# Performance work log

Measured on AMD Instinct MI355X. Metric: run time of the kernel, lower is better.

Reference implementation:

```python
import jax, jax.numpy as jnp
import numpy as np

H = 1024      # hidden_size
I = 512       # moe_intermediate_size
E = 8         # n_routed_experts
K = 2         # num_experts_per_tok
SI = I * 2    # shared expert intermediate (n_shared_experts=2)
B, S = 2, 1024


def setup_inputs() -> dict:
    key = jax.random.key(0)
    ks = jax.random.split(key, 9)
    s = 0.02
    return {
        "x": jax.random.normal(ks[0], (B, S, H), jnp.float32),
        "gate_w": jax.random.normal(ks[1], (E, H), jnp.float32) * s,
        "lb_bias": jnp.zeros((E,), jnp.float32),
        "expert_gate_w": jax.random.normal(ks[2], (E, I, H), jnp.float32) * s,
        "expert_up_w": jax.random.normal(ks[3], (E, I, H), jnp.float32) * s,
        "expert_down_w": jax.random.normal(ks[4], (E, H, I), jnp.float32) * s,
        "shared_gate_w": jax.random.normal(ks[5], (SI, H), jnp.float32) * s,
        "shared_up_w": jax.random.normal(ks[6], (SI, H), jnp.float32) * s,
        "shared_down_w": jax.random.normal(ks[7], (H, SI), jnp.float32) * s,
    }


def _mlp(x, gw, uw, dw):
    # SwiGLU: down( silu(gate(x)) * up(x) )
    return (jax.nn.silu(x @ gw.T) * (x @ uw.T)) @ dw.T


def reference(x, gate_w, lb_bias, expert_gate_w, expert_up_w, expert_down_w,
              shared_gate_w, shared_up_w, shared_down_w):
    b, s, h = x.shape
    xf = x.reshape(-1, h)                                   # [T, H]
    # --- SimpleRouter (sigmoid scoring) ---
    logits = xf @ gate_w.T + lb_bias                        # [T, E]
    scores = jax.nn.sigmoid(logits.astype(jnp.float32))
    topw, topi = jax.lax.top_k(scores, K)                   # [T, K]
    topw = (topw / (topw.sum(-1, keepdims=True) + 1e-8)).astype(x.dtype)
    # --- _process_local: per-expert dispatch/compute/combine ---
    # Faithful to torch source: expert_weights[mask].mean(dim=-1) collapses to a
    # SCALAR per expert (mean routing weight over all tokens sent to that expert).
    out = jnp.zeros_like(xf)
    for e in range(E):
        m = (topi == e)                                     # [T, K]
        sel = m.any(axis=-1)                                # [T]
        cnt = m.sum()
        wmean = (topw * m).sum() / jnp.maximum(cnt, 1).astype(topw.dtype)
        y = _mlp(xf, expert_gate_w[e], expert_up_w[e], expert_down_w[e])  # [T, H]
        out = out + jnp.where(sel[:, None], y * wmean, jnp.zeros((), x.dtype))
    out = out.reshape(b, s, h)
    # --- shared experts ---
    out = out + _mlp(x, shared_gate_w, shared_up_w, shared_down_w)
    return out
```

## Files before the change

### kernel.cpp

```cpp
#include <hip/hip_runtime.h>

#define H_DIM 1024
#define I_DIM 512
#define NE 8
#define SI_DIM 1024
#define NT 2048

typedef __bf16 bf16;
typedef __bf16 bf16x4 __attribute__((ext_vector_type(4)));
typedef __bf16 bf16x8 __attribute__((ext_vector_type(8)));
typedef float f32x4 __attribute__((ext_vector_type(4)));

#define W_GU 0ull
#define W_DN 8388608ull
#define W_SGU 12582912ull
#define W_SDN 14680064ull
#define W_TOT 15728640ull

#define NWB 15360
#define NRB 512

#define OFF_CNT 0
#define OFF_WM 64
#define OFF_TOPI 1024
#define OFF_TOPW (OFF_TOPI + NT * 8)
#define OFF_LISTS (OFF_TOPW + NT * 8)
#define OFF_WB (OFF_LISTS + NE * NT * 4)
#define OFF_XB (OFF_WB + (size_t)W_TOT * 2)
#define OFF_ACTE (OFF_XB + (size_t)NT * H_DIM * 2)
#define OFF_ACTS (OFF_ACTE + (size_t)NE * NT * I_DIM * 2)

__device__ __forceinline__ bf16x4 cvt4(f32x4 v) {
  bf16x4 r;
  r.x = (bf16)v.x; r.y = (bf16)v.y; r.z = (bf16)v.z; r.w = (bf16)v.w;
  return r;
}

__device__ __forceinline__ void glds16(const bf16* g, bf16* l) {
  __builtin_amdgcn_global_load_lds(
      (const __attribute__((address_space(1))) unsigned int*)g,
      (__attribute__((address_space(3))) unsigned int*)l, 16, 0, 0);
}

__global__ __launch_bounds__(256) void prep_kernel(
    const float* __restrict__ x, const float* __restrict__ gw,
    const float* __restrict__ lb, const float* __restrict__ eg,
    const float* __restrict__ eu, const float* __restrict__ ed,
    const float* __restrict__ sg, const float* __restrict__ su,
    const float* __restrict__ sd, bf16* __restrict__ wb,
    bf16* __restrict__ xb, int2* __restrict__ topi,
    float2* __restrict__ topw) {
  const int bx = blockIdx.x;
  const int tid = threadIdx.x;
  if (bx < NWB) {
    size_t i = ((size_t)bx * 256 + tid) * 4;
    const float* src;
    if (i < W_DN) {
      size_t z = i >> 20;
      int rem = (int)(i & ((1u << 20) - 1));
      int rp = rem >> 10, k = rem & 1023;
      int b = rp >> 4;
      int sr = ((b >> 1) << 4) | (rp & 15);
      src = ((b & 1) ? eu : eg) + (z << 19) + ((size_t)sr << 10) + k;
    } else if (i < W_SGU) {
      src = ed + (i - W_DN);
    } else if (i < W_SDN) {
      int rem = (int)(i - W_SGU);
      int rp = rem >> 10, k = rem & 1023;
      int b = rp >> 4;
      int sr = ((b >> 1) << 4) | (rp & 15);
      src = ((b & 1) ? su : sg) + ((size_t)sr << 10) + k;
    } else {
      src = sd + (i - W_SDN);
    }
    *(bf16x4*)(wb + i) = cvt4(*(const f32x4*)src);
  } else {
    const int lane = tid & 63;
    const int t = (bx - NWB) * 4 + (tid >> 6);
    const float* xr = x + (size_t)t * H_DIM;
    bf16* xw = xb + (size_t)t * H_DIM;
    float s[NE];
#pragma unroll
    for (int e = 0; e < NE; e++) s[e] = 0.f;
#pragma unroll
    for (int k0 = 0; k0 < H_DIM; k0 += 256) {
      f32x4 xv = *(const f32x4*)(xr + k0 + lane * 4);
      *(bf16x4*)(xw + k0 + lane * 4) = cvt4(xv);
#pragma unroll
      for (int e = 0; e < NE; e++) {
        f32x4 gv = *(const f32x4*)(gw + e * H_DIM + k0 + lane * 4);
        s[e] += xv.x * gv.x + xv.y * gv.y + xv.z * gv.z + xv.w * gv.w;
      }
    }
#pragma unroll
    for (int e = 0; e < NE; e++) {
      float v = s[e];
#pragma unroll
      for (int off = 32; off > 0; off >>= 1) v += __shfl_xor(v, off);
      s[e] = v;
    }
    if (lane == 0) {
      float sc[NE];
#pragma unroll
      for (int e = 0; e < NE; e++) sc[e] = 1.f / (1.f + expf(-(s[e] + lb[e])));
      int i1 = 0;
#pragma unroll
      for (int e = 1; e < NE; e++)
        if (sc[e] > sc[i1]) i1 = e;
      int i2 = -1;
#pragma unroll
      for (int e = 0; e < NE; e++) {
        if (e == i1) continue;
        if (i2 < 0 || sc[e] > sc[i2]) i2 = e;
      }
      float w1 = sc[i1], w2 = sc[i2];
      float inv = 1.f / (w1 + w2 + 1e-8f);
      topi[t] = make_int2(i1, i2);
      topw[t] = make_float2(w1 * inv, w2 * inv);
    }
  }
}

__global__ __launch_bounds__(256) void build_kernel(
    const int2* __restrict__ topi, const float2* __restrict__ topw,
    int* __restrict__ cnt, float* __restrict__ wm, int* __restrict__ lists) {
  const int e = blockIdx.x;
  const int wave = threadIdx.x >> 6, lane = threadIdx.x & 63;
  __shared__ int wc[4];
  __shared__ float wf[4];
  const int tbeg = wave * (NT / 4), tend = tbeg + NT / 4;

  int c = 0;
  float wa = 0.f;
  for (int t0 = tbeg; t0 < tend; t0 += 64) {
    int2 ti = topi[t0 + lane];
    float2 tw = topw[t0 + lane];
    bool hit = (ti.x == e) || (ti.y == e);
    float w = (ti.x == e) ? tw.x : ((ti.y == e) ? tw.y : 0.f);
    c += __popcll(__ballot(hit));
#pragma unroll
    for (int off = 32; off > 0; off >>= 1) w += __shfl_xor(w, off);
    wa += w;
  }
  if (lane == 0) { wc[wave] = c; wf[wave] = wa; }
  __syncthreads();
  int pos = 0;
  for (int w = 0; w < wave; w++) pos += wc[w];
  for (int t0 = tbeg; t0 < tend; t0 += 64) {
    int t = t0 + lane;
    int2 ti = topi[t];
    bool hit = (ti.x == e) || (ti.y == e);
    unsigned long long m = __ballot(hit);
    int pre = __popcll(m & ((1ull << lane) - 1ull));
    if (hit) lists[e * NT + pos + pre] = t;
    pos += __popcll(m);
  }
  if (threadIdx.x == 0) {
    int ctot = wc[0] + wc[1] + wc[2] + wc[3];
    cnt[e] = ctot;
    wm[e] = (wf[0] + wf[1] + wf[2] + wf[3]) / (float)(ctot > 0 ? ctot : 1);
  }
}

__global__ __launch_bounds__(256, 4) void gemm_gu(
    const bf16* __restrict__ wb, const bf16* __restrict__ xb,
    const int* __restrict__ cnt, const int* __restrict__ lists,
    bf16* __restrict__ act_e, bf16* __restrict__ act_s) {
  const int z = blockIdx.z, ct = blockIdx.x, rt = blockIdx.y;
  const int tid = threadIdx.x;
  __shared__ int rows_s[64];
  __shared__ __align__(16) bf16 As[64 * 64];
  __shared__ __align__(16) bf16 Bs[128 * 64];
  int mrem, ldc;
  bf16* Cb;
  const bf16* Bb;
  if (z < NE) {
    if (ct >= 8) return;
    int c = cnt[z];
    if (rt * 64 >= c) return;
    mrem = c - rt * 64;
    if (tid < 64)
      rows_s[tid] = lists[z * NT + rt * 64 + (tid < mrem ? tid : mrem - 1)];
    Bb = wb + W_GU + ((size_t)z << 20) + (size_t)ct * 128 * H_DIM;
    Cb = act_e + ((size_t)z * NT + rt * 64) * I_DIM;
    ldc = I_DIM;
  } else {
    mrem = 64;
    if (tid < 64) rows_s[tid] = rt * 64 + tid;
    Bb = wb + W_SGU + (size_t)ct * 128 * H_DIM;
    Cb = act_s + (size_t)rt * 64 * SI_DIM;
    ldc = SI_DIM;
  }
  __syncthreads();

  const int lane = tid & 63, wave = tid >> 6;
  const int mw = (wave & 1) * 32, nw = (wave >> 1) * 64;
  const int l15 = lane & 15, quad = lane >> 4;
  const int srow = tid >> 3;
  const int cch = tid & 7;
  const int p8 = cch * 8;
  const int sx = (l15 & 7) * 8;

  const bf16 *ap[2], *bp[4];
  int alo[2], blo[4];
#pragma unroll
  for (int r = 0; r < 2; r++) {
    int R = srow + r * 32;
    int gs = (cch ^ (R & 7)) * 8;
    ap[r] = xb + (size_t)rows_s[R] * H_DIM + gs;
    alo[r] = R * 64 + p8;
  }
#pragma unroll
  for (int r = 0; r < 4; r++) {
    int R = srow + r * 32;
    int gs = (cch ^ (R & 7)) * 8;
    bp[r] = Bb + (size_t)R * H_DIM + gs;
    blo[r] = R * 64 + p8;
  }

  f32x4 acc[2][4] = {};
  for (int k0 = 0; k0 < H_DIM; k0 += 64) {
#pragma unroll
    for (int r = 0; r < 2; r++) glds16(ap[r] + k0, &As[alo[r]]);
#pragma unroll
    for (int r = 0; r < 4; r++) glds16(bp[r] + k0, &Bs[blo[r]]);
    __syncthreads();
#pragma unroll
    for (int kk = 0; kk < 2; kk++) {
      const int ko = (kk * 4 + quad) * 8;
      bf16x8 av[2], bv[4];
#pragma unroll
      for (int i = 0; i < 2; i++)
        av[i] = *(const bf16x8*)&As[(mw + i * 16 + l15) * 64 + (ko ^ sx)];
#pragma unroll
      for (int j = 0; j < 4; j++)
        bv[j] = *(const bf16x8*)&Bs[(nw + j * 16 + l15) * 64 + (ko ^ sx)];
#pragma unroll
      for (int i = 0; i < 2; i++)
#pragma unroll
        for (int j = 0; j < 4; j++)
          acc[i][j] = __builtin_amdgcn_mfma_f32_16x16x32_bf16(av[i], bv[j], acc[i][j], 0, 0, 0);
    }
    __syncthreads();
  }

#pragma unroll
  for (int i = 0; i < 2; i++) {
#pragma unroll
    for (int rg = 0; rg < 4; rg++) {
      int rl = mw + i * 16 + quad * 4 + rg;
      if (rl < mrem) {
#pragma unroll
        for (int jp = 0; jp < 2; jp++) {
          float g = acc[i][jp * 2][rg];
          float u = acc[i][jp * 2 + 1][rg];
          int c = ct * 64 + (nw >> 1) + jp * 16 + l15;
          Cb[(size_t)rl * ldc + c] = (bf16)((g / (1.f + __expf(-g))) * u);
        }
      }
    }
  }
}

__global__ __launch_bounds__(256, 4) void gemm_down(
    const bf16* __restrict__ wb, const bf16* __restrict__ act_e,
    const bf16* __restrict__ act_s, const int* __restrict__ cnt,
    const float* __restrict__ wm, const int* __restrict__ lists,
    float* __restrict__ out) {
  const int z = blockIdx.z, ct = blockIdx.x, rt = blockIdx.y;
  const int tid = threadIdx.x;
  __shared__ int rows_s[64];
  __shared__ __align__(16) bf16 As[64 * 64];
  __shared__ __align__(16) bf16 Bs[128 * 64];
  int K, mrem;
  const bf16 *Ab, *Bb;
  if (z < NE) {
    int c = cnt[z];
    if (rt * 64 >= c) return;
    mrem = c - rt * 64;
    if (tid < 64)
      rows_s[tid] = lists[z * NT + rt * 64 + (tid < mrem ? tid : mrem - 1)];
    Ab = act_e + ((size_t)z * NT + rt * 64) * I_DIM;
    K = I_DIM;
    Bb = wb + W_DN + ((size_t)z << 19) + (size_t)ct * 128 * I_DIM;
  } else {
    mrem = 64;
    if (tid < 64) rows_s[tid] = rt * 64 + tid;
    Ab = act_s + (size_t)rt * 64 * SI_DIM;
    K = SI_DIM;
    Bb = wb + W_SDN + (size_t)ct * 128 * SI_DIM;
  }
  __syncthreads();

  const int lane = tid & 63, wave = tid >> 6;
  const int mw = (wave & 1) * 32, nw = (wave >> 1) * 64;
  const int l15 = lane & 15, quad = lane >> 4;
  const int srow = tid >> 3;
  const int cch = tid & 7;
  const int p8 = cch * 8;
  const int sx = (l15 & 7) * 8;

  const bf16 *ap[2], *bp[4];
  int alo[2], blo[4];
#pragma unroll
  for (int r = 0; r < 2; r++) {
    int R = srow + r * 32;
    int gs = (cch ^ (R & 7)) * 8;
    ap[r] = Ab + (size_t)R * K + gs;
    alo[r] = R * 64 + p8;
  }
#pragma unroll
  for (int r = 0; r < 4; r++) {
    int R = srow + r * 32;
    int gs = (cch ^ (R & 7)) * 8;
    bp[r] = Bb + (size_t)R * K + gs;
    blo[r] = R * 64 + p8;
  }

  f32x4 acc[2][4] = {};
  for (int k0 = 0; k0 < K; k0 += 64) {
#pragma unroll
    for (int r = 0; r < 2; r++) glds16(ap[r] + k0, &As[alo[r]]);
#pragma unroll
    for (int r = 0; r < 4; r++) glds16(bp[r] + k0, &Bs[blo[r]]);
    __syncthreads();
#pragma unroll
    for (int kk = 0; kk < 2; kk++) {
      const int ko = (kk * 4 + quad) * 8;
      bf16x8 av[2], bv[4];
#pragma unroll
      for (int i = 0; i < 2; i++)
        av[i] = *(const bf16x8*)&As[(mw + i * 16 + l15) * 64 + (ko ^ sx)];
#pragma unroll
      for (int j = 0; j < 4; j++)
        bv[j] = *(const bf16x8*)&Bs[(nw + j * 16 + l15) * 64 + (ko ^ sx)];
#pragma unroll
      for (int i = 0; i < 2; i++)
#pragma unroll
        for (int j = 0; j < 4; j++)
          acc[i][j] = __builtin_amdgcn_mfma_f32_16x16x32_bf16(av[i], bv[j], acc[i][j], 0, 0, 0);
    }
    __syncthreads();
  }

  const float wsc = (z < NE) ? wm[z] : 1.f;
#pragma unroll
  for (int i = 0; i < 2; i++) {
#pragma unroll
    for (int rg = 0; rg < 4; rg++) {
      int rl = mw + i * 16 + quad * 4 + rg;
      if (rl < mrem) {
        int t = rows_s[rl];
        float* orow = out + (size_t)t * H_DIM + ct * 128 + nw;
#pragma unroll
        for (int j = 0; j < 4; j++)
          atomicAdd(&orow[j * 16 + l15], wsc * acc[i][j][rg]);
      }
    }
  }
}

extern "C" void kernel_launch(void* const* d_in, const int* in_sizes, int n_in,
                              void* d_out, int out_size, void* d_ws,
                              size_t ws_size, hipStream_t stream) {
  (void)in_sizes; (void)n_in; (void)out_size; (void)ws_size;
  const float* x  = (const float*)d_in[0];
  const float* gw = (const float*)d_in[1];
  const float* lb = (const float*)d_in[2];
  const float* eg = (const float*)d_in[3];
  const float* eu = (const float*)d_in[4];
  const float* ed = (const float*)d_in[5];
  const float* sg = (const float*)d_in[6];
  const float* su = (const float*)d_in[7];
  const float* sd = (const float*)d_in[8];
  float* out = (float*)d_out;
  char* ws = (char*)d_ws;

  int* cnt     = (int*)(ws + OFF_CNT);
  float* wm    = (float*)(ws + OFF_WM);
  int2* topi   = (int2*)(ws + OFF_TOPI);
  float2* topw = (float2*)(ws + OFF_TOPW);
  int* lists   = (int*)(ws + OFF_LISTS);
  bf16* wb     = (bf16*)(ws + OFF_WB);
  bf16* xb     = (bf16*)(ws + OFF_XB);
  bf16* act_e  = (bf16*)(ws + OFF_ACTE);
  bf16* act_s  = (bf16*)(ws + OFF_ACTS);

  hipMemsetAsync(d_out, 0, (size_t)NT * H_DIM * sizeof(float), stream);
  prep_kernel<<<NWB + NRB, 256, 0, stream>>>(x, gw, lb, eg, eu, ed, sg, su, sd,
                                             wb, xb, topi, topw);
  build_kernel<<<NE, 256, 0, stream>>>(topi, topw, cnt, wm, lists);
  gemm_gu<<<dim3(16, 32, 9), 256, 0, stream>>>(wb, xb, cnt, lists, act_e,
                                               act_s);
  gemm_down<<<dim3(8, 32, 9), 256, 0, stream>>>(wb, act_e, act_s, cnt, wm,
                                                lists, out);
}
```

Baseline: 203.3 us.

## Fuse all MoE stages into one persistent kernel with grid barriers

Replaces the memset plus four kernel launches with a single persistent kernel of 1024 blocks. The blocks loop over the prep, routing-list, gate/up GEMM and down GEMM work units and separate the phases with atomic global barriers. Output zeroing moves into the first phase. This removes launch gaps and tail effects between stages, but needs all 1024 blocks co-resident (256 CUs at 4 blocks each) or the barrier deadlocks. It also loses the dynamic early exit of empty tiles, which now cost a loop iteration.

```diff
diff --git a/kernel.cpp b/kernel.cpp
--- a/kernel.cpp
+++ b/kernel.cpp
@@ -5,6 +5,7 @@
 #define NE 8
 #define SI_DIM 1024
 #define NT 2048
+#define GRID 1024
 
 typedef __bf16 bf16;
 typedef __bf16 bf16x4 __attribute__((ext_vector_type(4)));
@@ -19,6 +20,8 @@
 
 #define NWB 15360
 #define NRB 512
+#define NZB 2048
+#define NU (NWB + NRB + NZB)
 
 #define OFF_CNT 0
 #define OFF_WM 64
@@ -29,6 +32,7 @@
 #define OFF_XB (OFF_WB + (size_t)W_TOT * 2)
 #define OFF_ACTE (OFF_XB + (size_t)NT * H_DIM * 2)
 #define OFF_ACTS (OFF_ACTE + (size_t)NE * NT * I_DIM * 2)
+#define OFF_BAR (OFF_ACTS + (size_t)NT * SI_DIM * 2)
 
 __device__ __forceinline__ bf16x4 cvt4(f32x4 v) {
   bf16x4 r;
@@ -42,156 +46,151 @@
       (__attribute__((address_space(3))) unsigned int*)l, 16, 0, 0);
 }
 
-__global__ __launch_bounds__(256) void prep_kernel(
+__device__ __forceinline__ void gsync(unsigned* bar) {
+  __syncthreads();
+  if (threadIdx.x == 0) {
+    __threadfence();
+    __hip_atomic_fetch_add(bar, 1u, __ATOMIC_RELAXED, __HIP_MEMORY_SCOPE_AGENT);
+    while (__hip_atomic_load(bar, __ATOMIC_RELAXED, __HIP_MEMORY_SCOPE_AGENT) <
+           (unsigned)GRID) {
+      __builtin_amdgcn_s_sleep(4);
+    }
+    __threadfence();
+  }
+  __syncthreads();
+}
+
+__global__ __launch_bounds__(256, 4) void moe_kernel(
     const float* __restrict__ x, const float* __restrict__ gw,
     const float* __restrict__ lb, const float* __restrict__ eg,
     const float* __restrict__ eu, const float* __restrict__ ed,
     const float* __restrict__ sg, const float* __restrict__ su,
     const float* __restrict__ sd, bf16* __restrict__ wb,
     bf16* __restrict__ xb, int2* __restrict__ topi,
-    float2* __restrict__ topw) {
-  const int bx = blockIdx.x;
+    float2* __restrict__ topw, int* __restrict__ cnt,
+    float* __restrict__ wm, int* __restrict__ lists,
+    bf16* __restrict__ act_e, bf16* __restrict__ act_s,
+    float* __restrict__ out, unsigned* __restrict__ bar) {
   const int tid = threadIdx.x;
-  if (bx < NWB) {
-    size_t i = ((size_t)bx * 256 + tid) * 4;
-    const float* src;
-    if (i < W_DN) {
-      size_t z = i >> 20;
-      int rem = (int)(i & ((1u << 20) - 1));
-      int rp = rem >> 10, k = rem & 1023;
-      int b = rp >> 4;
-      int sr = ((b >> 1) << 4) | (rp & 15);
-      src = ((b & 1) ? eu : eg) + (z << 19) + ((size_t)sr << 10) + k;
-    } else if (i < W_SGU) {
-      src = ed + (i - W_DN);
-    } else if (i < W_SDN) {
-      int rem = (int)(i - W_SGU);
-      int rp = rem >> 10, k = rem & 1023;
-      int b = rp >> 4;
-      int sr = ((b >> 1) << 4) | (rp & 15);
-      src = ((b & 1) ? su : sg) + ((size_t)sr << 10) + k;
+  const int bid = blockIdx.x;
+  __shared__ __align__(16) char smem[24832];
+  bf16* As = (bf16*)smem;
+  bf16* Bs = (bf16*)(smem + 8192);
+  int* rows_s = (int*)(smem + 24576);
+
+  for (int u = bid; u < NU; u += GRID) {
+    if (u < NWB) {
+      size_t i = ((size_t)u * 256 + tid) * 4;
+      const float* src;
+      if (i < W_DN) {
+        size_t z = i >> 20;
+        int rem = (int)(i & ((1u << 20) - 1));
+        int rp = rem >> 10, k = rem & 1023;
+        int b = rp >> 4;
+        int sr = ((b >> 1) << 4) | (rp & 15);
+        src = ((b & 1) ? eu : eg) + (z << 19) + ((size_t)sr << 10) + k;
+      } else if (i < W_SGU) {
+        src = ed + (i - W_DN);
+      } else if (i < W_SDN) {
+        int rem = (int)(i - W_SGU);
+        int rp = rem >> 10, k = rem & 1023;
+        int b = rp >> 4;
+        int sr = ((b >> 1) << 4) | (rp & 15);
+        src = ((b & 1) ? su : sg) + ((size_t)sr << 10) + k;
+      } else {
+        src = sd + (i - W_SDN);
+      }
+      *(bf16x4*)(wb + i) = cvt4(*(const f32x4*)src);
+    } else if (u < NWB + NRB) {
+      const int lane = tid & 63;
+      const int t = (u - NWB) * 4 + (tid >> 6);
+      const float* xr = x + (size_t)t * H_DIM;
+      bf16* xw = xb + (size_t)t * H_DIM;
+      float s[NE];
+#pragma unroll
+      for (int e = 0; e < NE; e++) s[e] = 0.f;
+#pragma unroll
+      for (int k0 = 0; k0 < H_DIM; k0 += 256) {
+        f32x4 xv = *(const f32x4*)(xr + k0 + lane * 4);
+        *(bf16x4*)(xw + k0 + lane * 4) = cvt4(xv);
+#pragma unroll
+        for (int e = 0; e < NE; e++) {
+          f32x4 gv = *(const f32x4*)(gw + e * H_DIM + k0 + lane * 4);
+          s[e] += xv.x * gv.x + xv.y * gv.y + xv.z * gv.z + xv.w * gv.w;
+        }
+      }
+#pragma unroll
+      for (int e = 0; e < NE; e++) {
+        float v = s[e];
+#pragma unroll
+        for (int off = 32; off > 0; off >>= 1) v += __shfl_xor(v, off);
+        s[e] = v;
+      }
+      if (lane == 0) {
+        float sc[NE];
+#pragma unroll
+        for (int e = 0; e < NE; e++) sc[e] = 1.f / (1.f + expf(-(s[e] + lb[e])));
+        int i1 = 0;
+#pragma unroll
+        for (int e = 1; e < NE; e++)
+          if (sc[e] > sc[i1]) i1 = e;
+        int i2 = -1;
+#pragma unroll
+        for (int e = 0; e < NE; e++) {
+          if (e == i1) continue;
+          if (i2 < 0 || sc[e] > sc[i2]) i2 = e;
+        }
+        float w1 = sc[i1], w2 = sc[i2];
+        float inv = 1.f / (w1 + w2 + 1e-8f);
+        topi[t] = make_int2(i1, i2);
+        topw[t] = make_float2(w1 * inv, w2 * inv);
+      }
     } else {
-      src = sd + (i - W_SDN);
-    }
-    *(bf16x4*)(wb + i) = cvt4(*(const f32x4*)src);
-  } else {
-    const int lane = tid & 63;
-    const int t = (bx - NWB) * 4 + (tid >> 6);
-    const float* xr = x + (size_t)t * H_DIM;
-    bf16* xw = xb + (size_t)t * H_DIM;
-    float s[NE];
-#pragma unroll
-    for (int e = 0; e < NE; e++) s[e] = 0.f;
-#pragma unroll
-    for (int k0 = 0; k0 < H_DIM; k0 += 256) {
-      f32x4 xv = *(const f32x4*)(xr + k0 + lane * 4);
-      *(bf16x4*)(xw + k0 + lane * 4) = cvt4(xv);
-#pragma unroll
-      for (int e = 0; e < NE; e++) {
-        f32x4 gv = *(const f32x4*)(gw + e * H_DIM + k0 + lane * 4);
-        s[e] += xv.x * gv.x + xv.y * gv.y + xv.z * gv.z + xv.w * gv.w;
-      }
-    }
-#pragma unroll
-    for (int e = 0; e < NE; e++) {
-      float v = s[e];
-#pragma unroll
-      for (int off = 32; off > 0; off >>= 1) v += __shfl_xor(v, off);
-      s[e] = v;
-    }
-    if (lane == 0) {
-      float sc[NE];
-#pragma unroll
-      for (int e = 0; e < NE; e++) sc[e] = 1.f / (1.f + expf(-(s[e] + lb[e])));
-      int i1 = 0;
-#pragma unroll
-      for (int e = 1; e < NE; e++)
-        if (sc[e] > sc[i1]) i1 = e;
-      int i2 = -1;
-#pragma unroll
-      for (int e = 0; e < NE; e++) {
-        if (e == i1) continue;
-        if (i2 < 0 || sc[e] > sc[i2]) i2 = e;
-      }
-      float w1 = sc[i1], w2 = sc[i2];
-      float inv = 1.f / (w1 + w2 + 1e-8f);
-      topi[t] = make_int2(i1, i2);
-      topw[t] = make_float2(w1 * inv, w2 * inv);
+      size_t j = ((size_t)(u - NWB - NRB) * 256 + tid) * 4;
+      f32x4 zz = {0.f, 0.f, 0.f, 0.f};
+      *(f32x4*)(out + j) = zz;
     }
   }
-}
-
-__global__ __launch_bounds__(256) void build_kernel(
-    const int2* __restrict__ topi, const float2* __restrict__ topw,
-    int* __restrict__ cnt, float* __restrict__ wm, int* __restrict__ lists) {
-  const int e = blockIdx.x;
-  const int wave = threadIdx.x >> 6, lane = threadIdx.x & 63;
-  __shared__ int wc[4];
-  __shared__ float wf[4];
-  const int tbeg = wave * (NT / 4), tend = tbeg + NT / 4;
-
-  int c = 0;
-  float wa = 0.f;
-  for (int t0 = tbeg; t0 < tend; t0 += 64) {
-    int2 ti = topi[t0 + lane];
-    float2 tw = topw[t0 + lane];
-    bool hit = (ti.x == e) || (ti.y == e);
-    float w = (ti.x == e) ? tw.x : ((ti.y == e) ? tw.y : 0.f);
-    c += __popcll(__ballot(hit));
-#pragma unroll
-    for (int off = 32; off > 0; off >>= 1) w += __shfl_xor(w, off);
-    wa += w;
+  gsync(bar + 0);
+
+  if (bid < NE) {
+    const int e = bid;
+    const int wave = tid >> 6, lane = tid & 63;
+    int* wc = rows_s;
+    float* wf = (float*)(rows_s + 8);
+    const int tbeg = wave * (NT / 4), tend = tbeg + NT / 4;
+    int c = 0;
+    float wa = 0.f;
+    for (int t0 = tbeg; t0 < tend; t0 += 64) {
+      int2 ti = topi[t0 + lane];
+      float2 tw = topw[t0 + lane];
+      bool hit = (ti.x == e) || (ti.y == e);
+      float w = (ti.x == e) ? tw.x : ((ti.y == e) ? tw.y : 0.f);
+      c += __popcll(__ballot(hit));
+#pragma unroll
+      for (int off = 32; off > 0; off >>= 1) w += __shfl_xor(w, off);
+      wa += w;
+    }
+    if (lane == 0) { wc[wave] = c; wf[wave] = wa; }
+    __syncthreads();
+    int pos = 0;
+    for (int w = 0; w < wave; w++) pos += wc[w];
+    for (int t0 = tbeg; t0 < tend; t0 += 64) {
+      int t = t0 + lane;
+      int2 ti = topi[t];
+      bool hit = (ti.x == e) || (ti.y == e);
+      unsigned long long m = __ballot(hit);
+      int pre = __popcll(m & ((1ull << lane) - 1ull));
+      if (hit) lists[e * NT + pos + pre] = t;
+      pos += __popcll(m);
+    }
+    if (tid == 0) {
+      int ctot = wc[0] + wc[1] + wc[2] + wc[3];
+      cnt[e] = ctot;
+      wm[e] = (wf[0] + wf[1] + wf[2] + wf[3]) / (float)(ctot > 0 ? ctot : 1);
+    }
   }
-  if (lane == 0) { wc[wave] = c; wf[wave] = wa; }
-  __syncthreads();
-  int pos = 0;
-  for (int w = 0; w < wave; w++) pos += wc[w];
-  for (int t0 = tbeg; t0 < tend; t0 += 64) {
-    int t = t0 + lane;
-    int2 ti = topi[t];
-    bool hit = (ti.x == e) || (ti.y == e);
-    unsigned long long m = __ballot(hit);
-    int pre = __popcll(m & ((1ull << lane) - 1ull));
-    if (hit) lists[e * NT + pos + pre] = t;
-    pos += __popcll(m);
-  }
-  if (threadIdx.x == 0) {
-    int ctot = wc[0] + wc[1] + wc[2] + wc[3];
-    cnt[e] = ctot;
-    wm[e] = (wf[0] + wf[1] + wf[2] + wf[3]) / (float)(ctot > 0 ? ctot : 1);
-  }
-}
-
-__global__ __launch_bounds__(256, 4) void gemm_gu(
-    const bf16* __restrict__ wb, const bf16* __restrict__ xb,
-    const int* __restrict__ cnt, const int* __restrict__ lists,
-    bf16* __restrict__ act_e, bf16* __restrict__ act_s) {
-  const int z = blockIdx.z, ct = blockIdx.x, rt = blockIdx.y;
-  const int tid = threadIdx.x;
-  __shared__ int rows_s[64];
-  __shared__ __align__(16) bf16 As[64 * 64];
-  __shared__ __align__(16) bf16 Bs[128 * 64];
-  int mrem, ldc;
-  bf16* Cb;
-  const bf16* Bb;
-  if (z < NE) {
-    if (ct >= 8) return;
-    int c = cnt[z];
-    if (rt * 64 >= c) return;
-    mrem = c - rt * 64;
-    if (tid < 64)
-      rows_s[tid] = lists[z * NT + rt * 64 + (tid < mrem ? tid : mrem - 1)];
-    Bb = wb + W_GU + ((size_t)z << 20) + (size_t)ct * 128 * H_DIM;
-    Cb = act_e + ((size_t)z * NT + rt * 64) * I_DIM;
-    ldc = I_DIM;
-  } else {
-    mrem = 64;
-    if (tid < 64) rows_s[tid] = rt * 64 + tid;
-    Bb = wb + W_SGU + (size_t)ct * 128 * H_DIM;
-    Cb = act_s + (size_t)rt * 64 * SI_DIM;
-    ldc = SI_DIM;
-  }
-  __syncthreads();
+  gsync(bar + 16);
 
   const int lane = tid & 63, wave = tid >> 6;
   const int mw = (wave & 1) * 32, nw = (wave >> 1) * 64;
@@ -201,162 +200,175 @@
   const int p8 = cch * 8;
   const int sx = (l15 & 7) * 8;
 
-  const bf16 *ap[2], *bp[4];
-  int alo[2], blo[4];
-#pragma unroll
-  for (int r = 0; r < 2; r++) {
-    int R = srow + r * 32;
-    int gs = (cch ^ (R & 7)) * 8;
-    ap[r] = xb + (size_t)rows_s[R] * H_DIM + gs;
-    alo[r] = R * 64 + p8;
-  }
-#pragma unroll
-  for (int r = 0; r < 4; r++) {
-    int R = srow + r * 32;
-    int gs = (cch ^ (R & 7)) * 8;
-    bp[r] = Bb + (size_t)R * H_DIM + gs;
-    blo[r] = R * 64 + p8;
-  }
-
-  f32x4 acc[2][4] = {};
-  for (int k0 = 0; k0 < H_DIM; k0 += 64) {
-#pragma unroll
-    for (int r = 0; r < 2; r++) glds16(ap[r] + k0, &As[alo[r]]);
-#pragma unroll
-    for (int r = 0; r < 4; r++) glds16(bp[r] + k0, &Bs[blo[r]]);
+  for (int vb = bid; vb < 2560; vb += GRID) {
+    int z, ct, rt;
+    if (vb < 512) { z = NE; ct = vb & 15; rt = vb >> 4; }
+    else { int r0 = vb - 512; z = r0 & 7; ct = (r0 >> 3) & 7; rt = r0 >> 6; }
+    int mrem, ldc;
+    bf16* Cb;
+    const bf16* Bb;
+    if (z < NE) {
+      int c = cnt[z];
+      if (rt * 64 >= c) continue;
+      mrem = c - rt * 64;
+      Bb = wb + W_GU + ((size_t)z << 20) + (size_t)ct * 128 * H_DIM;
+      Cb = act_e + ((size_t)z * NT + rt * 64) * I_DIM;
+      ldc = I_DIM;
+    } else {
+      mrem = 64;
+      Bb = wb + W_SGU + (size_t)ct * 128 * H_DIM;
+      Cb = act_s + (size_t)rt * 64 * SI_DIM;
+      ldc = SI_DIM;
+    }
+    if (tid < 64)
+      rows_s[tid] = (z < NE)
+          ? lists[z * NT + rt * 64 + (tid < mrem ? tid : mrem - 1)]
+          : rt * 64 + tid;
     __syncthreads();
-#pragma unroll
-    for (int kk = 0; kk < 2; kk++) {
-      const int ko = (kk * 4 + quad) * 8;
-      bf16x8 av[2], bv[4];
-#pragma unroll
-      for (int i = 0; i < 2; i++)
-        av[i] = *(const bf16x8*)&As[(mw + i * 16 + l15) * 64 + (ko ^ sx)];
-#pragma unroll
-      for (int j = 0; j < 4; j++)
-        bv[j] = *(const bf16x8*)&Bs[(nw + j * 16 + l15) * 64 + (ko ^ sx)];
-#pragma unroll
-      for (int i = 0; i < 2; i++)
+    const bf16 *ap[2], *bp[4];
+    int alo[2], blo[4];
+#pragma unroll
+    for (int r = 0; r < 2; r++) {
+      int R = srow + r * 32;
+      int gs = (cch ^ (R & 7)) * 8;
+      ap[r] = xb + (size_t)rows_s[R] * H_DIM + gs;
+      alo[r] = R * 64 + p8;
+    }
+#pragma unroll
+    for (int r = 0; r < 4; r++) {
+      int R = srow + r * 32;
+      int gs = (cch ^ (R & 7)) * 8;
+      bp[r] = Bb + (size_t)R * H_DIM + gs;
+      blo[r] = R * 64 + p8;
+    }
+    f32x4 acc[2][4] = {};
+    for (int k0 = 0; k0 < H_DIM; k0 += 64) {
+#pragma unroll
+      for (int r = 0; r < 2; r++) glds16(ap[r] + k0, &As[alo[r]]);
+#pragma unroll
+      for (int r = 0; r < 4; r++) glds16(bp[r] + k0, &Bs[blo[r]]);
+      __syncthreads();
+#pragma unroll
+      for (int kk = 0; kk < 2; kk++) {
+        const int ko = (kk * 4 + quad) * 8;
+        bf16x8 av[2], bv[4];
+#pragma unroll
+        for (int i = 0; i < 2; i++)
+          av[i] = *(const bf16x8*)&As[(mw + i * 16 + l15) * 64 + (ko ^ sx)];
 #pragma unroll
         for (int j = 0; j < 4; j++)
-          acc[i][j] = __builtin_amdgcn_mfma_f32_16x16x32_bf16(av[i], bv[j], acc[i][j], 0, 0, 0);
+          bv[j] = *(const bf16x8*)&Bs[(nw + j * 16 + l15) * 64 + (ko ^ sx)];
+#pragma unroll
+        for (int i = 0; i < 2; i++)
+#pragma unroll
+          for (int j = 0; j < 4; j++)
+            acc[i][j] = __builtin_amdgcn_mfma_f32_16x16x32_bf16(
+                av[i], bv[j], acc[i][j], 0, 0, 0);
+      }
+      __syncthreads();
+    }
+#pragma unroll
+    for (int i = 0; i < 2; i++) {
+#pragma unroll
+      for (int rg = 0; rg < 4; rg++) {
+        int rl = mw + i * 16 + quad * 4 + rg;
+        if (rl < mrem) {
+#pragma unroll
+          for (int jp = 0; jp < 2; jp++) {
+            float g = acc[i][jp * 2][rg];
+            float u = acc[i][jp * 2 + 1][rg];
+            int c = ct * 64 + (nw >> 1) + jp * 16 + l15;
+            Cb[(size_t)rl * ldc + c] = (bf16)((g / (1.f + __expf(-g))) * u);
+          }
+        }
+      }
     }
     __syncthreads();
   }
-
-#pragma unroll
-  for (int i = 0; i < 2; i++) {
-#pragma unroll
-    for (int rg = 0; rg < 4; rg++) {
-      int rl = mw + i * 16 + quad * 4 + rg;
-      if (rl < mrem) {
-#pragma unroll
-        for (int jp = 0; jp < 2; jp++) {
-          float g = acc[i][jp * 2][rg];
-          float u = acc[i][jp * 2 + 1][rg];
-          int c = ct * 64 + (nw >> 1) + jp * 16 + l15;
-          Cb[(size_t)rl * ldc + c] = (bf16)((g / (1.f + __expf(-g))) * u);
+  gsync(bar + 32);
+
+  for (int vb = bid; vb < 2304; vb += GRID) {
+    int z, ct, rt;
+    if (vb < 256) { z = NE; ct = vb & 7; rt = vb >> 3; }
+    else { int r0 = vb - 256; z = r0 & 7; ct = (r0 >> 3) & 7; rt = r0 >> 6; }
+    int K, mrem;
+    const bf16 *Ab, *Bb;
+    if (z < NE) {
+      int c = cnt[z];
+      if (rt * 64 >= c) continue;
+      mrem = c - rt * 64;
+      Ab = act_e + ((size_t)z * NT + rt * 64) * I_DIM;
+      K = I_DIM;
+      Bb = wb + W_DN + ((size_t)z << 19) + (size_t)ct * 128 * I_DIM;
+    } else {
+      mrem = 64;
+      Ab = act_s + (size_t)rt * 64 * SI_DIM;
+      K = SI_DIM;
+      Bb = wb + W_SDN + (size_t)ct * 128 * SI_DIM;
+    }
+    if (tid < 64)
+      rows_s[tid] = (z < NE)
+          ? lists[z * NT + rt * 64 + (tid < mrem ? tid : mrem - 1)]
+          : rt * 64 + tid;
+    __syncthreads();
+    const bf16 *ap[2], *bp[4];
+    int alo[2], blo[4];
+#pragma unroll
+    for (int r = 0; r < 2; r++) {
+      int R = srow + r * 32;
+      int gs = (cch ^ (R & 7)) * 8;
+      ap[r] = Ab + (size_t)R * K + gs;
+      alo[r] = R * 64 + p8;
+    }
+#pragma unroll
+    for (int r = 0; r < 4; r++) {
+      int R = srow + r * 32;
+      int gs = (cch ^ (R & 7)) * 8;
+      bp[r] = Bb + (size_t)R * K + gs;
+      blo[r] = R * 64 + p8;
+    }
+    f32x4 acc[2][4] = {};
+    for (int k0 = 0; k0 < K; k0 += 64) {
+#pragma unroll
+      for (int r = 0; r < 2; r++) glds16(ap[r] + k0, &As[alo[r]]);
+#pragma unroll
+      for (int r = 0; r < 4; r++) glds16(bp[r] + k0, &Bs[blo[r]]);
+      __syncthreads();
+#pragma unroll
+      for (int kk = 0; kk < 2; kk++) {
+        const int ko = (kk * 4 + quad) * 8;
+        bf16x8 av[2], bv[4];
+#pragma unroll
+        for (int i = 0; i < 2; i++)
+          av[i] = *(const bf16x8*)&As[(mw + i * 16 + l15) * 64 + (ko ^ sx)];
+#pragma unroll
+        for (int j = 0; j < 4; j++)
+          bv[j] = *(const bf16x8*)&Bs[(nw + j * 16 + l15) * 64 + (ko ^ sx)];
+#pragma unroll
+        for (int i = 0; i < 2; i++)
+#pragma unroll
+          for (int j = 0; j < 4; j++)
+            acc[i][j] = __builtin_amdgcn_mfma_f32_16x16x32_bf16(
+                av[i], bv[j], acc[i][j], 0, 0, 0);
+      }
+      __syncthreads();
+    }
+    const float wsc = (z < NE) ? wm[z] : 1.f;
+#pragma unroll
+    for (int i = 0; i < 2; i++) {
+#pragma unroll
+      for (int rg = 0; rg < 4; rg++) {
+        int rl = mw + i * 16 + quad * 4 + rg;
+        if (rl < mrem) {
+          int t = rows_s[rl];
+          float* orow = out + (size_t)t * H_DIM + ct * 128 + nw;
+#pragma unroll
+          for (int j = 0; j < 4; j++)
+            atomicAdd(&orow[j * 16 + l15], wsc * acc[i][j][rg]);
         }
       }
     }
-  }
-}
-
-__global__ __launch_bounds__(256, 4) void gemm_down(
-    const bf16* __restrict__ wb, const bf16* __restrict__ act_e,
-    const bf16* __restrict__ act_s, const int* __restrict__ cnt,
-    const float* __restrict__ wm, const int* __restrict__ lists,
-    float* __restrict__ out) {
-  const int z = blockIdx.z, ct = blockIdx.x, rt = blockIdx.y;
-  const int tid = threadIdx.x;
-  __shared__ int rows_s[64];
-  __shared__ __align__(16) bf16 As[64 * 64];
-  __shared__ __align__(16) bf16 Bs[128 * 64];
-  int K, mrem;
-  const bf16 *Ab, *Bb;
-  if (z < NE) {
-    int c = cnt[z];
-    if (rt * 64 >= c) return;
-    mrem = c - rt * 64;
-    if (tid < 64)
-      rows_s[tid] = lists[z * NT + rt * 64 + (tid < mrem ? tid : mrem - 1)];
-    Ab = act_e + ((size_t)z * NT + rt * 64) * I_DIM;
-    K = I_DIM;
-    Bb = wb + W_DN + ((size_t)z << 19) + (size_t)ct * 128 * I_DIM;
-  } else {
-    mrem = 64;
-    if (tid < 64) rows_s[tid] = rt * 64 + tid;
-    Ab = act_s + (size_t)rt * 64 * SI_DIM;
-    K = SI_DIM;
-    Bb = wb + W_SDN + (size_t)ct * 128 * SI_DIM;
-  }
-  __syncthreads();
-
-  const int lane = tid & 63, wave = tid >> 6;
-  const int mw = (wave & 1) * 32, nw = (wave >> 1) * 64;
-  const int l15 = lane & 15, quad = lane >> 4;
-  const int srow = tid >> 3;
-  const int cch = tid & 7;
-  const int p8 = cch * 8;
-  const int sx = (l15 & 7) * 8;
-
-  const bf16 *ap[2], *bp[4];
-  int alo[2], blo[4];
-#pragma unroll
-  for (int r = 0; r < 2; r++) {
-    int R = srow + r * 32;
-    int gs = (cch ^ (R & 7)) * 8;
-    ap[r] = Ab + (size_t)R * K + gs;
-    alo[r] = R * 64 + p8;
-  }
-#pragma unroll
-  for (int r = 0; r < 4; r++) {
-    int R = srow + r * 32;
-    int gs = (cch ^ (R & 7)) * 8;
-    bp[r] = Bb + (size_t)R * K + gs;
-    blo[r] = R * 64 + p8;
-  }
-
-  f32x4 acc[2][4] = {};
-  for (int k0 = 0; k0 < K; k0 += 64) {
-#pragma unroll
-    for (int r = 0; r < 2; r++) glds16(ap[r] + k0, &As[alo[r]]);
-#pragma unroll
-    for (int r = 0; r < 4; r++) glds16(bp[r] + k0, &Bs[blo[r]]);
     __syncthreads();
-#pragma unroll
-    for (int kk = 0; kk < 2; kk++) {
-      const int ko = (kk * 4 + quad) * 8;
-      bf16x8 av[2], bv[4];
-#pragma unroll
-      for (int i = 0; i < 2; i++)
-        av[i] = *(const bf16x8*)&As[(mw + i * 16 + l15) * 64 + (ko ^ sx)];
-#pragma unroll
-      for (int j = 0; j < 4; j++)
-        bv[j] = *(const bf16x8*)&Bs[(nw + j * 16 + l15) * 64 + (ko ^ sx)];
-#pragma unroll
-      for (int i = 0; i < 2; i++)
-#pragma unroll
-        for (int j = 0; j < 4; j++)
-          acc[i][j] = __builtin_amdgcn_mfma_f32_16x16x32_bf16(av[i], bv[j], acc[i][j], 0, 0, 0);
-    }
-    __syncthreads();
-  }
-
-  const float wsc = (z < NE) ? wm[z] : 1.f;
-#pragma unroll
-  for (int i = 0; i < 2; i++) {
-#pragma unroll
-    for (int rg = 0; rg < 4; rg++) {
-      int rl = mw + i * 16 + quad * 4 + rg;
-      if (rl < mrem) {
-        int t = rows_s[rl];
-        float* orow = out + (size_t)t * H_DIM + ct * 128 + nw;
-#pragma unroll
-        for (int j = 0; j < 4; j++)
-          atomicAdd(&orow[j * 16 + l15], wsc * acc[i][j][rg]);
-      }
-    }
   }
 }
 
@@ -385,13 +397,10 @@
   bf16* xb     = (bf16*)(ws + OFF_XB);
   bf16* act_e  = (bf16*)(ws + OFF_ACTE);
   bf16* act_s  = (bf16*)(ws + OFF_ACTS);
-
-  hipMemsetAsync(d_out, 0, (size_t)NT * H_DIM * sizeof(float), stream);
-  prep_kernel<<<NWB + NRB, 256, 0, stream>>>(x, gw, lb, eg, eu, ed, sg, su, sd,
-                                             wb, xb, topi, topw);
-  build_kernel<<<NE, 256, 0, stream>>>(topi, topw, cnt, wm, lists);
-  gemm_gu<<<dim3(16, 32, 9), 256, 0, stream>>>(wb, xb, cnt, lists, act_e,
-                                               act_s);
-  gemm_down<<<dim3(8, 32, 9), 256, 0, stream>>>(wb, act_e, act_s, cnt, wm,
-                                                lists, out);
+  unsigned* bar = (unsigned*)(ws + OFF_BAR);
+
+  hipMemsetAsync(bar, 0, 256, stream);
+  moe_kernel<<<GRID, 256, 0, stream>>>(x, gw, lb, eg, eu, ed, sg, su, sd, wb,
+                                       xb, topi, topw, cnt, wm, lists, act_e,
+                                       act_s, out, bar);
 }
```

Measured after the change: 516.6 us. +154.1%, slower.

## Fold memset and list build into other kernels, use compact persistent-style GEMM grids

Applied to the files above, without the earlier changes.

Removes the separate memset and build_kernel launches. Output zeroing moves into extra blocks of prep_kernel, and each GEMM block rebuilds its expert's token list in shared memory from topi. Both GEMMs now use flat grids sized to a fixed number of blocks that loop over row tiles with a stride, so no blocks launch only to exit early. In exchange, every block redundantly scans all 2048 tokens with a single wave before it starts computing, and the launch_bounds occupancy hint is dropped.

```diff
diff --git a/kernel.cpp b/kernel.cpp
--- a/kernel.cpp
+++ b/kernel.cpp
@@ -19,6 +19,7 @@
 
 #define NWB 15360
 #define NRB 512
+#define NZB 2048
 
 #define OFF_CNT 0
 #define OFF_WM 64
@@ -49,7 +50,7 @@
     const float* __restrict__ sg, const float* __restrict__ su,
     const float* __restrict__ sd, bf16* __restrict__ wb,
     bf16* __restrict__ xb, int2* __restrict__ topi,
-    float2* __restrict__ topw) {
+    float2* __restrict__ topw, float* __restrict__ out) {
   const int bx = blockIdx.x;
   const int tid = threadIdx.x;
   if (bx < NWB) {
@@ -74,7 +75,7 @@
       src = sd + (i - W_SDN);
     }
     *(bf16x4*)(wb + i) = cvt4(*(const f32x4*)src);
-  } else {
+  } else if (bx < NWB + NRB) {
     const int lane = tid & 63;
     const int t = (bx - NWB) * 4 + (tid >> 6);
     const float* xr = x + (size_t)t * H_DIM;
@@ -118,82 +119,52 @@
       topi[t] = make_int2(i1, i2);
       topw[t] = make_float2(w1 * inv, w2 * inv);
     }
-  }
-}
-
-__global__ __launch_bounds__(256) void build_kernel(
-    const int2* __restrict__ topi, const float2* __restrict__ topw,
-    int* __restrict__ cnt, float* __restrict__ wm, int* __restrict__ lists) {
-  const int e = blockIdx.x;
-  const int wave = threadIdx.x >> 6, lane = threadIdx.x & 63;
-  __shared__ int wc[4];
-  __shared__ float wf[4];
-  const int tbeg = wave * (NT / 4), tend = tbeg + NT / 4;
-
-  int c = 0;
-  float wa = 0.f;
-  for (int t0 = tbeg; t0 < tend; t0 += 64) {
-    int2 ti = topi[t0 + lane];
-    float2 tw = topw[t0 + lane];
-    bool hit = (ti.x == e) || (ti.y == e);
-    float w = (ti.x == e) ? tw.x : ((ti.y == e) ? tw.y : 0.f);
-    c += __popcll(__ballot(hit));
-#pragma unroll
-    for (int off = 32; off > 0; off >>= 1) w += __shfl_xor(w, off);
-    wa += w;
-  }
-  if (lane == 0) { wc[wave] = c; wf[wave] = wa; }
-  __syncthreads();
-  int pos = 0;
-  for (int w = 0; w < wave; w++) pos += wc[w];
-  for (int t0 = tbeg; t0 < tend; t0 += 64) {
-    int t = t0 + lane;
-    int2 ti = topi[t];
-    bool hit = (ti.x == e) || (ti.y == e);
-    unsigned long long m = __ballot(hit);
-    int pre = __popcll(m & ((1ull << lane) - 1ull));
-    if (hit) lists[e * NT + pos + pre] = t;
-    pos += __popcll(m);
-  }
-  if (threadIdx.x == 0) {
-    int ctot = wc[0] + wc[1] + wc[2] + wc[3];
-    cnt[e] = ctot;
-    wm[e] = (wf[0] + wf[1] + wf[2] + wf[3]) / (float)(ctot > 0 ? ctot : 1);
-  }
-}
-
-__global__ __launch_bounds__(256, 4) void gemm_gu(
+  } else {
+    size_t j = ((size_t)(bx - NWB - NRB) * 256 + tid) * 4;
+    f32x4 zz = {0.f, 0.f, 0.f, 0.f};
+    *(f32x4*)(out + j) = zz;
+  }
+}
+
+__global__ __launch_bounds__(256) void gemm_gu(
     const bf16* __restrict__ wb, const bf16* __restrict__ xb,
-    const int* __restrict__ cnt, const int* __restrict__ lists,
-    bf16* __restrict__ act_e, bf16* __restrict__ act_s) {
-  const int z = blockIdx.z, ct = blockIdx.x, rt = blockIdx.y;
+    const int2* __restrict__ topi, bf16* __restrict__ act_e,
+    bf16* __restrict__ act_s) {
+  const int b = blockIdx.x;
   const int tid = threadIdx.x;
-  __shared__ int rows_s[64];
+  const int lane = tid & 63, wave = tid >> 6;
   __shared__ __align__(16) bf16 As[64 * 64];
   __shared__ __align__(16) bf16 Bs[128 * 64];
-  int mrem, ldc;
-  bf16* Cb;
-  const bf16* Bb;
+  __shared__ int list_s[NT];
+  __shared__ int cnt_s;
+
+  int z, ct, rt0, rstride;
+  if (b < 1024) {
+    z = b & 7; ct = (b >> 3) & 7; rt0 = b >> 6; rstride = 16;
+  } else {
+    int s = b - 1024; z = NE; ct = s & 15; rt0 = s >> 4; rstride = 32;
+  }
+
   if (z < NE) {
-    if (ct >= 8) return;
-    int c = cnt[z];
-    if (rt * 64 >= c) return;
-    mrem = c - rt * 64;
-    if (tid < 64)
-      rows_s[tid] = lists[z * NT + rt * 64 + (tid < mrem ? tid : mrem - 1)];
-    Bb = wb + W_GU + ((size_t)z << 20) + (size_t)ct * 128 * H_DIM;
-    Cb = act_e + ((size_t)z * NT + rt * 64) * I_DIM;
-    ldc = I_DIM;
+    if (wave == 0) {
+      int pos = 0;
+      for (int t0 = 0; t0 < NT; t0 += 64) {
+        int2 ti = topi[t0 + lane];
+        bool hit = (ti.x == z) || (ti.y == z);
+        unsigned long long m = __ballot(hit);
+        int pre = __popcll(m & ((1ull << lane) - 1ull));
+        if (hit) list_s[pos + pre] = t0 + lane;
+        pos += __popcll(m);
+      }
+      if (lane == 0) cnt_s = pos;
+    }
   } else {
-    mrem = 64;
-    if (tid < 64) rows_s[tid] = rt * 64 + tid;
-    Bb = wb + W_SGU + (size_t)ct * 128 * H_DIM;
-    Cb = act_s + (size_t)rt * 64 * SI_DIM;
-    ldc = SI_DIM;
+    for (int i = tid; i < NT; i += 256) list_s[i] = i;
+    if (tid == 0) cnt_s = NT;
   }
   __syncthreads();
-
-  const int lane = tid & 63, wave = tid >> 6;
+  const int c = cnt_s;
+
   const int mw = (wave & 1) * 32, nw = (wave >> 1) * 64;
   const int l15 = lane & 15, quad = lane >> 4;
   const int srow = tid >> 3;
@@ -201,15 +172,14 @@
   const int p8 = cch * 8;
   const int sx = (l15 & 7) * 8;
 
-  const bf16 *ap[2], *bp[4];
-  int alo[2], blo[4];
-#pragma unroll
-  for (int r = 0; r < 2; r++) {
-    int R = srow + r * 32;
-    int gs = (cch ^ (R & 7)) * 8;
-    ap[r] = xb + (size_t)rows_s[R] * H_DIM + gs;
-    alo[r] = R * 64 + p8;
-  }
+  const bf16* Bb = (z < NE)
+      ? wb + W_GU + ((size_t)z << 20) + (size_t)ct * 128 * H_DIM
+      : wb + W_SGU + (size_t)ct * 128 * H_DIM;
+  bf16* Cbase = (z < NE) ? act_e + (size_t)z * NT * I_DIM : act_s;
+  const int ldc = (z < NE) ? I_DIM : SI_DIM;
+
+  const bf16* bp[4];
+  int blo[4];
 #pragma unroll
   for (int r = 0; r < 4; r++) {
     int R = srow + r * 32;
@@ -218,81 +188,116 @@
     blo[r] = R * 64 + p8;
   }
 
-  f32x4 acc[2][4] = {};
-  for (int k0 = 0; k0 < H_DIM; k0 += 64) {
-#pragma unroll
-    for (int r = 0; r < 2; r++) glds16(ap[r] + k0, &As[alo[r]]);
-#pragma unroll
-    for (int r = 0; r < 4; r++) glds16(bp[r] + k0, &Bs[blo[r]]);
-    __syncthreads();
-#pragma unroll
-    for (int kk = 0; kk < 2; kk++) {
-      const int ko = (kk * 4 + quad) * 8;
-      bf16x8 av[2], bv[4];
-#pragma unroll
-      for (int i = 0; i < 2; i++)
-        av[i] = *(const bf16x8*)&As[(mw + i * 16 + l15) * 64 + (ko ^ sx)];
-#pragma unroll
-      for (int j = 0; j < 4; j++)
-        bv[j] = *(const bf16x8*)&Bs[(nw + j * 16 + l15) * 64 + (ko ^ sx)];
-#pragma unroll
-      for (int i = 0; i < 2; i++)
+  for (int rtv = rt0; rtv * 64 < c; rtv += rstride) {
+    const int mr = c - rtv * 64;
+    const int gmr = mr < 64 ? mr : 64;
+    const bf16* ap[2];
+    int alo[2];
+#pragma unroll
+    for (int r = 0; r < 2; r++) {
+      int R = srow + r * 32;
+      int gs = (cch ^ (R & 7)) * 8;
+      int row = list_s[rtv * 64 + (R < gmr ? R : gmr - 1)];
+      ap[r] = xb + (size_t)row * H_DIM + gs;
+      alo[r] = R * 64 + p8;
+    }
+    f32x4 acc[2][4] = {};
+    for (int k0 = 0; k0 < H_DIM; k0 += 64) {
+#pragma unroll
+      for (int r = 0; r < 2; r++) glds16(ap[r] + k0, &As[alo[r]]);
+#pragma unroll
+      for (int r = 0; r < 4; r++) glds16(bp[r] + k0, &Bs[blo[r]]);
+      __syncthreads();
+#pragma unroll
+      for (int kk = 0; kk < 2; kk++) {
+        const int ko = (kk * 4 + quad) * 8;
+        bf16x8 av[2], bv[4];
+#pragma unroll
+        for (int i = 0; i < 2; i++)
+          av[i] = *(const bf16x8*)&As[(mw + i * 16 + l15) * 64 + (ko ^ sx)];
 #pragma unroll
         for (int j = 0; j < 4; j++)
-          acc[i][j] = __builtin_amdgcn_mfma_f32_16x16x32_bf16(av[i], bv[j], acc[i][j], 0, 0, 0);
-    }
-    __syncthreads();
-  }
-
-#pragma unroll
-  for (int i = 0; i < 2; i++) {
-#pragma unroll
-    for (int rg = 0; rg < 4; rg++) {
-      int rl = mw + i * 16 + quad * 4 + rg;
-      if (rl < mrem) {
-#pragma unroll
-        for (int jp = 0; jp < 2; jp++) {
-          float g = acc[i][jp * 2][rg];
-          float u = acc[i][jp * 2 + 1][rg];
-          int c = ct * 64 + (nw >> 1) + jp * 16 + l15;
-          Cb[(size_t)rl * ldc + c] = (bf16)((g / (1.f + __expf(-g))) * u);
+          bv[j] = *(const bf16x8*)&Bs[(nw + j * 16 + l15) * 64 + (ko ^ sx)];
+#pragma unroll
+        for (int i = 0; i < 2; i++)
+#pragma unroll
+          for (int j = 0; j < 4; j++)
+            acc[i][j] = __builtin_amdgcn_mfma_f32_16x16x32_bf16(
+                av[i], bv[j], acc[i][j], 0, 0, 0);
+      }
+      __syncthreads();
+    }
+    bf16* Cb = Cbase + (size_t)rtv * 64 * ldc;
+#pragma unroll
+    for (int i = 0; i < 2; i++) {
+#pragma unroll
+      for (int rg = 0; rg < 4; rg++) {
+        int rl = mw + i * 16 + quad * 4 + rg;
+        if (rl < gmr) {
+#pragma unroll
+          for (int jp = 0; jp < 2; jp++) {
+            float g = acc[i][jp * 2][rg];
+            float u = acc[i][jp * 2 + 1][rg];
+            int cc = ct * 64 + (nw >> 1) + jp * 16 + l15;
+            Cb[(size_t)rl * ldc + cc] = (bf16)((g / (1.f + __expf(-g))) * u);
+          }
         }
       }
     }
   }
 }
 
-__global__ __launch_bounds__(256, 4) void gemm_down(
+__global__ __launch_bounds__(256) void gemm_down(
     const bf16* __restrict__ wb, const bf16* __restrict__ act_e,
-    const bf16* __restrict__ act_s, const int* __restrict__ cnt,
-    const float* __restrict__ wm, const int* __restrict__ lists,
-    float* __restrict__ out) {
-  const int z = blockIdx.z, ct = blockIdx.x, rt = blockIdx.y;
+    const bf16* __restrict__ act_s, const int2* __restrict__ topi,
+    const float2* __restrict__ topw, float* __restrict__ out) {
+  const int b = blockIdx.x;
   const int tid = threadIdx.x;
-  __shared__ int rows_s[64];
+  const int lane = tid & 63, wave = tid >> 6;
   __shared__ __align__(16) bf16 As[64 * 64];
   __shared__ __align__(16) bf16 Bs[128 * 64];
-  int K, mrem;
-  const bf16 *Ab, *Bb;
+  __shared__ int list_s[NT];
+  __shared__ int cnt_s;
+  __shared__ float wm_s;
+
+  int z, ct, rt0, rstride;
+  if (b < 1024) {
+    z = b & 7; ct = (b >> 3) & 7; rt0 = b >> 6; rstride = 16;
+  } else {
+    int s = b - 1024; z = NE; ct = s & 7; rt0 = s >> 3; rstride = 32;
+  }
+
   if (z < NE) {
-    int c = cnt[z];
-    if (rt * 64 >= c) return;
-    mrem = c - rt * 64;
-    if (tid < 64)
-      rows_s[tid] = lists[z * NT + rt * 64 + (tid < mrem ? tid : mrem - 1)];
-    Ab = act_e + ((size_t)z * NT + rt * 64) * I_DIM;
-    K = I_DIM;
-    Bb = wb + W_DN + ((size_t)z << 19) + (size_t)ct * 128 * I_DIM;
+    if (wave == 0) {
+      int pos = 0;
+      float wacc = 0.f;
+      for (int t0 = 0; t0 < NT; t0 += 64) {
+        int2 ti = topi[t0 + lane];
+        float2 tw = topw[t0 + lane];
+        bool hit = (ti.x == z) || (ti.y == z);
+        unsigned long long m = __ballot(hit);
+        int pre = __popcll(m & ((1ull << lane) - 1ull));
+        if (hit) {
+          list_s[pos + pre] = t0 + lane;
+          wacc += (ti.x == z) ? tw.x : tw.y;
+        }
+        pos += __popcll(m);
+      }
+#pragma unroll
+      for (int off = 32; off > 0; off >>= 1) wacc += __shfl_xor(wacc, off);
+      if (lane == 0) {
+        cnt_s = pos;
+        wm_s = wacc / (float)(pos > 0 ? pos : 1);
+      }
+    }
   } else {
-    mrem = 64;
-    if (tid < 64) rows_s[tid] = rt * 64 + tid;
-    Ab = act_s + (size_t)rt * 64 * SI_DIM;
-    K = SI_DIM;
-    Bb = wb + W_SDN + (size_t)ct * 128 * SI_DIM;
+    for (int i = tid; i < NT; i += 256) list_s[i] = i;
+    if (tid == 0) { cnt_s = NT; wm_s = 1.f; }
   }
   __syncthreads();
-
-  const int lane = tid & 63, wave = tid >> 6;
+  const int c = cnt_s;
+  const float wsc = wm_s;
+
   const int mw = (wave & 1) * 32, nw = (wave >> 1) * 64;
   const int l15 = lane & 15, quad = lane >> 4;
   const int srow = tid >> 3;
@@ -300,15 +305,14 @@
   const int p8 = cch * 8;
   const int sx = (l15 & 7) * 8;
 
-  const bf16 *ap[2], *bp[4];
-  int alo[2], blo[4];
-#pragma unroll
-  for (int r = 0; r < 2; r++) {
-    int R = srow + r * 32;
-    int gs = (cch ^ (R & 7)) * 8;
-    ap[r] = Ab + (size_t)R * K + gs;
-    alo[r] = R * 64 + p8;
-  }
+  const int K = (z < NE) ? I_DIM : SI_DIM;
+  const bf16* Bb = (z < NE)
+      ? wb + W_DN + ((size_t)z << 19) + (size_t)ct * 128 * I_DIM
+      : wb + W_SDN + (size_t)ct * 128 * SI_DIM;
+  const bf16* Abase = (z < NE) ? act_e + (size_t)z * NT * I_DIM : act_s;
+
+  const bf16* bp[4];
+  int blo[4];
 #pragma unroll
   for (int r = 0; r < 4; r++) {
     int R = srow + r * 32;
@@ -317,44 +321,57 @@
     blo[r] = R * 64 + p8;
   }
 
-  f32x4 acc[2][4] = {};
-  for (int k0 = 0; k0 < K; k0 += 64) {
-#pragma unroll
-    for (int r = 0; r < 2; r++) glds16(ap[r] + k0, &As[alo[r]]);
-#pragma unroll
-    for (int r = 0; r < 4; r++) glds16(bp[r] + k0, &Bs[blo[r]]);
-    __syncthreads();
-#pragma unroll
-    for (int kk = 0; kk < 2; kk++) {
-      const int ko = (kk * 4 + quad) * 8;
-      bf16x8 av[2], bv[4];
-#pragma unroll
-      for (int i = 0; i < 2; i++)
-        av[i] = *(const bf16x8*)&As[(mw + i * 16 + l15) * 64 + (ko ^ sx)];
-#pragma unroll
-      for (int j = 0; j < 4; j++)
-        bv[j] = *(const bf16x8*)&Bs[(nw + j * 16 + l15) * 64 + (ko ^ sx)];
-#pragma unroll
-      for (int i = 0; i < 2; i++)
+  for (int rtv = rt0; rtv * 64 < c; rtv += rstride) {
+    const int mr = c - rtv * 64;
+    const int gmr = mr < 64 ? mr : 64;
+    const bf16* Ab = Abase + (size_t)rtv * 64 * K;
+    const bf16* ap[2];
+    int alo[2];
+#pragma unroll
+    for (int r = 0; r < 2; r++) {
+      int R = srow + r * 32;
+      int gs = (cch ^ (R & 7)) * 8;
+      ap[r] = Ab + (size_t)R * K + gs;
+      alo[r] = R * 64 + p8;
+    }
+    f32x4 acc[2][4] = {};
+    for (int k0 = 0; k0 < K; k0 += 64) {
+#pragma unroll
+      for (int r = 0; r < 2; r++) glds16(ap[r] + k0, &As[alo[r]]);
+#pragma unroll
+      for (int r = 0; r < 4; r++) glds16(bp[r] + k0, &Bs[blo[r]]);
+      __syncthreads();
+#pragma unroll
+      for (int kk = 0; kk < 2; kk++) {
+        const int ko = (kk * 4 + quad) * 8;
+        bf16x8 av[2], bv[4];
+#pragma unroll
+        for (int i = 0; i < 2; i++)
+          av[i] = *(const bf16x8*)&As[(mw + i * 16 + l15) * 64 + (ko ^ sx)];
 #pragma unroll
         for (int j = 0; j < 4; j++)
-          acc[i][j] = __builtin_amdgcn_mfma_f32_16x16x32_bf16(av[i], bv[j], acc[i][j], 0, 0, 0);
-    }
-    __syncthreads();
-  }
-
-  const float wsc = (z < NE) ? wm[z] : 1.f;
-#pragma unroll
-  for (int i = 0; i < 2; i++) {
-#pragma unroll
-    for (int rg = 0; rg < 4; rg++) {
-      int rl = mw + i * 16 + quad * 4 + rg;
-      if (rl < mrem) {
-        int t = rows_s[rl];
-        float* orow = out + (size_t)t * H_DIM + ct * 128 + nw;
-#pragma unroll
-        for (int j = 0; j < 4; j++)
-          atomicAdd(&orow[j * 16 + l15], wsc * acc[i][j][rg]);
+          bv[j] = *(const bf16x8*)&Bs[(nw + j * 16 + l15) * 64 + (ko ^ sx)];
+#pragma unroll
+        for (int i = 0; i < 2; i++)
+#pragma unroll
+          for (int j = 0; j < 4; j++)
+            acc[i][j] = __builtin_amdgcn_mfma_f32_16x16x32_bf16(
+                av[i], bv[j], acc[i][j], 0, 0, 0);
+      }
+      __syncthreads();
+    }
+#pragma unroll
+    for (int i = 0; i < 2; i++) {
+#pragma unroll
+      for (int rg = 0; rg < 4; rg++) {
+        int rl = mw + i * 16 + quad * 4 + rg;
+        if (rl < gmr) {
+          int t = list_s[rtv * 64 + rl];
+          float* orow = out + (size_t)t * H_DIM + ct * 128 + nw;
+#pragma unroll
+          for (int j = 0; j < 4; j++)
+            atomicAdd(&orow[j * 16 + l15], wsc * acc[i][j][rg]);
+        }
       }
     }
   }
@@ -376,22 +393,16 @@
   float* out = (float*)d_out;
   char* ws = (char*)d_ws;
 
-  int* cnt     = (int*)(ws + OFF_CNT);
-  float* wm    = (float*)(ws + OFF_WM);
   int2* topi   = (int2*)(ws + OFF_TOPI);
   float2* topw = (float2*)(ws + OFF_TOPW);
-  int* lists   = (int*)(ws + OFF_LISTS);
   bf16* wb     = (bf16*)(ws + OFF_WB);
   bf16* xb     = (bf16*)(ws + OFF_XB);
   bf16* act_e  = (bf16*)(ws + OFF_ACTE);
   bf16* act_s  = (bf16*)(ws + OFF_ACTS);
 
-  hipMemsetAsync(d_out, 0, (size_t)NT * H_DIM * sizeof(float), stream);
-  prep_kernel<<<NWB + NRB, 256, 0, stream>>>(x, gw, lb, eg, eu, ed, sg, su, sd,
-                                             wb, xb, topi, topw);
-  build_kernel<<<NE, 256, 0, stream>>>(topi, topw, cnt, wm, lists);
-  gemm_gu<<<dim3(16, 32, 9), 256, 0, stream>>>(wb, xb, cnt, lists, act_e,
-                                               act_s);
-  gemm_down<<<dim3(8, 32, 9), 256, 0, stream>>>(wb, act_e, act_s, cnt, wm,
-                                                lists, out);
-}
+  prep_kernel<<<NWB + NRB + NZB, 256, 0, stream>>>(x, gw, lb, eg, eu, ed, sg,
+                                                   su, sd, wb, xb, topi, topw,
+                                                   out);
+  gemm_gu<<<1536, 256, 0, stream>>>(wb, xb, topi, act_e, act_s);
+  gemm_down<<<1280, 256, 0, stream>>>(wb, act_e, act_s, topi, topw, out);
+}
```

Result: slower. 215.9 us (+6.2%).
